# Optimization experiments

Measured on AMD Instinct MI355X. Metric: run time of the kernel, lower is better.

Reference implementation:

```python
import jax, jax.numpy as jnp
import numpy as np

B, T, D, H = 4, 2048, 1024, 16
HD = D // H  # head_dim = 64


def setup_inputs() -> dict:
    key = jax.random.key(0)
    ks = jax.random.split(key, 5)
    s = 0.02
    return {
        "x": jax.random.normal(ks[0], (B, T, D), dtype=jnp.float32),
        "Wq": jax.random.normal(ks[1], (D, D), dtype=jnp.float32) * s,
        "Wk": jax.random.normal(ks[2], (D, D), dtype=jnp.float32) * s,
        "Wv": jax.random.normal(ks[3], (D, D), dtype=jnp.float32) * s,
        "Wp": jax.random.normal(ks[4], (D, D), dtype=jnp.float32) * s,
    }


def reference(x, Wq, Wk, Wv, Wp):
    b, t, d = x.shape
    # QKV projections (bias=False), reshape to (b, h, t, hd)
    q = (x @ Wq.T).reshape(b, t, H, HD).transpose(0, 2, 1, 3)
    k = (x @ Wk.T).reshape(b, t, H, HD).transpose(0, 2, 1, 3)
    v = (x @ Wv.T).reshape(b, t, H, HD).transpose(0, 2, 1, 3)
    # scaled scores with causal mask
    scores = jnp.einsum("bhqd,bhkd->bhqk", q, k) / jnp.sqrt(jnp.float32(HD))
    causal = jnp.triu(jnp.ones((t, t), dtype=bool), k=1)
    scores = jnp.where(causal, -jnp.inf, scores)
    weights = jax.nn.softmax(scores, axis=-1)
    # dropout = 0.0 / eval mode -> identity
    ctx = jnp.einsum("bhqk,bhkd->bhqd", weights, v)
    ctx = ctx.transpose(0, 2, 1, 3).reshape(b, t, d)
    return ctx @ Wp.T
```

## Files before the change

kernel.cpp:

```cpp
#include <hip/hip_runtime.h>

typedef unsigned short u16;
typedef unsigned int u32;
typedef __attribute__((ext_vector_type(8))) short short8;
typedef __attribute__((ext_vector_type(4))) short short4_t;
typedef __attribute__((ext_vector_type(4))) float float4_t;

#define T_SEQ 2048
#define DMODEL 1024
#define NH 16
#define HD 64
#define NEG_BIG (-3.0e4f)

#define GLL16(g, l) __builtin_amdgcn_global_load_lds( \
    (const __attribute__((address_space(1))) u32*)(g), \
    (__attribute__((address_space(3))) u32*)(l), 16, 0, 0)

__device__ inline u16 f2b(float f) {
  u32 x = __builtin_bit_cast(u32, f);
  x += 0x7fffu + ((x >> 16) & 1u);
  return (u16)(x >> 16);
}

__global__ __launch_bounds__(256) void conv_f2b(
    const float* __restrict__ x, const float* __restrict__ wq,
    const float* __restrict__ wk, const float* __restrict__ wv,
    const float* __restrict__ wp, u16* __restrict__ xb, u16* __restrict__ wb) {
  const size_t SZc = (size_t)8192 * 1024, WSZc = (size_t)1024 * 1024;
  size_t i = ((size_t)blockIdx.x * 256 + threadIdx.x) * 8;
  const float* s; u16* d; size_t off;
  if (i < SZc) { s = x; d = xb; off = i; }
  else {
    size_t j = i - SZc;
    size_t w = j >> 20;
    off = j & (WSZc - 1);
    s = (w == 0) ? wq : (w == 1) ? wk : (w == 2) ? wv : wp;
    d = wb + w * WSZc;
  }
  float4_t a = *(const float4_t*)(s + off);
  float4_t b = *(const float4_t*)(s + off + 4);
  short8 o;
  o[0] = (short)f2b(a[0]); o[1] = (short)f2b(a[1]);
  o[2] = (short)f2b(a[2]); o[3] = (short)f2b(a[3]);
  o[4] = (short)f2b(b[0]); o[5] = (short)f2b(b[1]);
  o[6] = (short)f2b(b[2]); o[7] = (short)f2b(b[3]);
  *(short8*)(d + off) = o;
}

__global__ __launch_bounds__(256) void gemm_bt(
    const u16* __restrict__ A,
    const u16* __restrict__ B0, const u16* __restrict__ B1, const u16* __restrict__ B2,
    u16* __restrict__ C0, u16* __restrict__ C1, u16* __restrict__ C2,
    float* __restrict__ Cf,
    int N, int Kd, int vtz, int of32, int scz, float cscale)
{
  const u16* Bp = (blockIdx.z == 0) ? B0 : ((blockIdx.z == 1) ? B1 : B2);
  u16* Cp = (blockIdx.z == 0) ? C0 : ((blockIdx.z == 1) ? C1 : C2);
  const bool vt = ((int)blockIdx.z == vtz);
  const float cs = ((int)blockIdx.z == scz) ? cscale : 1.0f;
  __shared__ u16 As[128 * 32];
  __shared__ u16 Bs[128 * 32];
  const int tid = threadIdx.x;
  const int lane = tid & 63;
  const int li = lane & 15;
  const int quad = lane >> 4;
  const int wv = tid >> 6;
  const int wm = (wv >> 1) * 64;
  const int wn = (wv & 1) * 64;
  const size_t bm = (size_t)blockIdx.x * 128;
  const size_t bn = (size_t)blockIdx.y * 128;

  float4_t acc[4][4];
  const float4_t z4 = {0.f, 0.f, 0.f, 0.f};
#pragma unroll
  for (int i = 0; i < 4; i++)
#pragma unroll
    for (int j = 0; j < 4; j++) acc[i][j] = z4;

  const int c0 = tid, c1 = tid + 256;
  const int r0 = c0 >> 2, e0 = (c0 & 3) * 8;
  const int r1 = c1 >> 2, e1 = (c1 & 3) * 8;

  for (int k0 = 0; k0 < Kd; k0 += 32) {
    __syncthreads();
    GLL16(A + (bm + r0) * Kd + k0 + e0, &As[c0 * 8]);
    GLL16(A + (bm + r1) * Kd + k0 + e1, &As[c1 * 8]);
    GLL16(Bp + (bn + r0) * Kd + k0 + e0, &Bs[c0 * 8]);
    GLL16(Bp + (bn + r1) * Kd + k0 + e1, &Bs[c1 * 8]);
    __syncthreads();
    short8 af[4], bf[4];
#pragma unroll
    for (int i = 0; i < 4; i++)
      af[i] = *(const short8*)&As[(wm + i * 16 + li) * 32 + quad * 8];
#pragma unroll
    for (int j = 0; j < 4; j++)
      bf[j] = *(const short8*)&Bs[(wn + j * 16 + li) * 32 + quad * 8];
#pragma unroll
    for (int i = 0; i < 4; i++)
#pragma unroll
      for (int j = 0; j < 4; j++)
        acc[i][j] = __builtin_amdgcn_mfma_f32_16x16x32_bf16(af[i], bf[j], acc[i][j], 0, 0, 0);
  }

  if (of32) {
#pragma unroll
    for (int i = 0; i < 4; i++)
#pragma unroll
      for (int j = 0; j < 4; j++) {
        size_t row = bm + wm + (size_t)(i * 16 + quad * 4);
        size_t col = bn + wn + (size_t)(j * 16 + li);
#pragma unroll
        for (int r = 0; r < 4; r++)
          Cf[(row + r) * (size_t)N + col] = acc[i][j][r];
      }
  } else if (!vt) {
#pragma unroll
    for (int i = 0; i < 4; i++)
#pragma unroll
      for (int j = 0; j < 4; j++) {
        size_t row = bm + wm + (size_t)(i * 16 + quad * 4);
        size_t col = bn + wn + (size_t)(j * 16 + li);
#pragma unroll
        for (int r = 0; r < 4; r++)
          Cp[(row + r) * (size_t)N + col] = f2b(acc[i][j][r] * cs);
      }
  } else {
#pragma unroll
    for (int i = 0; i < 4; i++)
#pragma unroll
      for (int j = 0; j < 4; j++) {
        size_t row = bm + wm + (size_t)(i * 16 + quad * 4);
        size_t col = bn + wn + (size_t)(j * 16 + li);
        size_t bb = row >> 11;
        size_t tt = row & 2047;
        short4_t o;
#pragma unroll
        for (int r = 0; r < 4; r++) o[r] = (short)f2b(acc[i][j][r]);
        *(short4_t*)&Cp[(bb * 1024 + col) * 2048 + tt] = o;
      }
  }
}

#define LROW 72
__global__ __launch_bounds__(512) void attn_fwd(const u16* __restrict__ Qb,
                                                const u16* __restrict__ Kb,
                                                const u16* __restrict__ Vtb,
                                                u16* __restrict__ Ob) {
  __shared__ u16 Qs[128 * LROW];
  __shared__ u16 Ks[64 * LROW];
  __shared__ u16 Vs[64 * LROW];
  const int bh = blockIdx.y;
  const int bidx = bh >> 4;
  const int tid = threadIdx.x;
  const int lane = tid & 63;
  const int wv = tid >> 6;
  const int li = lane & 15;
  const int quad = lane >> 4;
  const size_t qkBase = ((size_t)bidx * T_SEQ) * DMODEL + (size_t)(bh & 15) * HD;
  const size_t vBase = (size_t)bh * HD * T_SEQ;
  const int krow = tid >> 3;
  const int kc8 = (tid & 7) * 8;
  const float4_t z4 = {0.f, 0.f, 0.f, 0.f};

#pragma unroll 1
  for (int ph = 0; ph < 2; ph++) {
    const int qblk = ph ? (int)blockIdx.x : (15 - (int)blockIdx.x);
    const int q0 = qblk * 128;

#pragma unroll
    for (int t = 0; t < 4; t++) {
      int slot = tid + t * 512;
      int row = slot >> 4, hc = slot & 15;
      *(short4_t*)&Qs[row * LROW + hc * 4] =
          *(const short4_t*)&Qb[qkBase + (size_t)(q0 + row) * DMODEL + hc * 4];
    }
    __syncthreads();
    short8 qf[2];
    {
      const int row = wv * 16 + li;
#pragma unroll
      for (int s = 0; s < 2; s++)
        qf[s] = *(const short8*)&Qs[row * LROW + s * 32 + quad * 8];
    }

    float4_t accO[4];
#pragma unroll
    for (int dt = 0; dt < 4; dt++) accO[dt] = z4;
    float l_i = 0.f;
    const int ktmax = 2 * qblk + 1;
    const int qg0 = q0 + wv * 16;

    short8 kpre = *(const short8*)&Kb[qkBase + (size_t)krow * DMODEL + kc8];
    short8 vpre = *(const short8*)&Vtb[vBase + (size_t)krow * T_SEQ + kc8];

    for (int kt = 0; kt <= ktmax; kt++) {
      const int k0 = kt * 64;
      __syncthreads();
      *(short8*)&Ks[krow * LROW + kc8] = kpre;
      *(short8*)&Vs[krow * LROW + kc8] = vpre;
      __syncthreads();
      if (kt < ktmax) {
        const int kn = k0 + 64;
        kpre = *(const short8*)&Kb[qkBase + (size_t)(kn + krow) * DMODEL + kc8];
        vpre = *(const short8*)&Vtb[vBase + (size_t)krow * T_SEQ + kn + kc8];
      }
      if (k0 > qg0 + 15) continue;

      float4_t st[4];
#pragma unroll
      for (int jt = 0; jt < 4; jt++) {
        float4_t c4 = z4;
        const int row = jt * 16 + li;
#pragma unroll
        for (int s = 0; s < 2; s++) {
          short8 kf = *(const short8*)&Ks[row * LROW + s * 32 + quad * 8];
          c4 = __builtin_amdgcn_mfma_f32_16x16x32_bf16(kf, qf[s], c4, 0, 0, 0);
        }
        st[jt] = c4;
      }

      float psum = 0.f;
      short4_t pf[4];
      if (k0 + 63 > qg0) {
        const int ig = qg0 + li;
#pragma unroll
        for (int jt = 0; jt < 4; jt++)
#pragma unroll
          for (int r = 0; r < 4; r++) {
            int jg = k0 + jt * 16 + quad * 4 + r;
            float p = (jg <= ig) ? __builtin_amdgcn_exp2f(st[jt][r]) : 0.f;
            psum += p;
            pf[jt][r] = (short)(__builtin_bit_cast(u32, p) >> 16);
          }
      } else {
#pragma unroll
        for (int jt = 0; jt < 4; jt++)
#pragma unroll
          for (int r = 0; r < 4; r++) {
            float p = __builtin_amdgcn_exp2f(st[jt][r]);
            psum += p;
            pf[jt][r] = (short)(__builtin_bit_cast(u32, p) >> 16);
          }
      }
      psum += __shfl_xor(psum, 16);
      psum += __shfl_xor(psum, 32);
      l_i += psum;

#pragma unroll
      for (int dt = 0; dt < 4; dt++) {
        const int d = dt * 16 + li;
#pragma unroll
        for (int jt = 0; jt < 4; jt++) {
          short4_t vf = *(const short4_t*)&Vs[d * LROW + jt * 16 + quad * 4];
          accO[dt] = __builtin_amdgcn_mfma_f32_16x16x16bf16_1k(vf, pf[jt], accO[dt], 0, 0, 0);
        }
      }
    }

    const float inv = 1.f / l_i;
    const int orow = q0 + wv * 16 + li;
    const size_t obase = ((size_t)bidx * T_SEQ + orow) * DMODEL + (size_t)(bh & 15) * HD;
#pragma unroll
    for (int dt = 0; dt < 4; dt++) {
      short4_t o4;
#pragma unroll
      for (int r = 0; r < 4; r++) o4[r] = (short)f2b(accO[dt][r] * inv);
      *(short4_t*)&Ob[obase + dt * 16 + quad * 4] = o4;
    }
  }
}

extern "C" void kernel_launch(void* const* d_in, const int* in_sizes, int n_in,
                              void* d_out, int out_size, void* d_ws, size_t ws_size,
                              hipStream_t stream) {
  (void)in_sizes; (void)n_in; (void)out_size; (void)ws_size;
  const float* x  = (const float*)d_in[0];
  const float* Wq = (const float*)d_in[1];
  const float* Wk = (const float*)d_in[2];
  const float* Wv = (const float*)d_in[3];
  const float* Wp = (const float*)d_in[4];
  float* out = (float*)d_out;

  const size_t SZ  = (size_t)8192 * 1024;
  const size_t WSZ = (size_t)1024 * 1024;

  u16* xb  = (u16*)d_ws;
  u16* wb  = xb + SZ;
  u16* Q   = wb + 4 * WSZ;
  u16* Kp  = Q + SZ;
  u16* Vt  = Kp + SZ;
  u16* ctx = Vt + SZ;

  const float SC = 0.18033688011112042f;

  dim3 blk(256);
  conv_f2b<<<dim3((unsigned)((SZ + 4 * WSZ) / 8 / 256)), blk, 0, stream>>>(
      x, Wq, Wk, Wv, Wp, xb, wb);
  gemm_bt<<<dim3(64, 8, 3), blk, 0, stream>>>(
      xb, wb, wb + WSZ, wb + 2 * WSZ, Q, Kp, Vt, nullptr, DMODEL, DMODEL, 2, 0,
      0, SC);
  attn_fwd<<<dim3(8, 4 * NH), dim3(512), 0, stream>>>(Q, Kp, Vt, ctx);
  gemm_bt<<<dim3(64, 8, 1), blk, 0, stream>>>(
      ctx, wb + 3 * WSZ, nullptr, nullptr, nullptr, nullptr, nullptr, out,
      DMODEL, DMODEL, -1, 1, -1, 1.0f);
}
```

Measured before the change: 256.2 us.

## Double-buffer K/V tiles in LDS and defer row-sum shuffle reduction

The attention kernel now keeps two LDS buffers for K and V tiles. The next tile is written into the alternate buffer while the current one is consumed, which removes one of the two block barriers per key-tile iteration. The per-iteration cross-lane shuffle reduction of the softmax denominator is also moved out of the loop and done once before normalization. The cost is double the K/V shared memory footprint, which could lower occupancy, plus an extra prologue load stage per phase.

```diff
diff --git a/kernel.cpp b/kernel.cpp
--- a/kernel.cpp
+++ b/kernel.cpp
@@ -10,7 +10,6 @@
 #define DMODEL 1024
 #define NH 16
 #define HD 64
-#define NEG_BIG (-3.0e4f)
 
 #define GLL16(g, l) __builtin_amdgcn_global_load_lds( \
     (const __attribute__((address_space(1))) u32*)(g), \
@@ -147,8 +146,8 @@
                                                 const u16* __restrict__ Vtb,
                                                 u16* __restrict__ Ob) {
   __shared__ u16 Qs[128 * LROW];
-  __shared__ u16 Ks[64 * LROW];
-  __shared__ u16 Vs[64 * LROW];
+  __shared__ u16 Kds[2][64 * LROW];
+  __shared__ u16 Vds[2][64 * LROW];
   const int bh = blockIdx.y;
   const int bidx = bh >> 4;
   const int tid = threadIdx.x;
@@ -160,13 +159,17 @@
   const size_t vBase = (size_t)bh * HD * T_SEQ;
   const int krow = tid >> 3;
   const int kc8 = (tid & 7) * 8;
+  const int kld = krow * LROW + kc8;
   const float4_t z4 = {0.f, 0.f, 0.f, 0.f};
 
 #pragma unroll 1
   for (int ph = 0; ph < 2; ph++) {
     const int qblk = ph ? (int)blockIdx.x : (15 - (int)blockIdx.x);
     const int q0 = qblk * 128;
-
+    const int ktmax = 2 * qblk + 1;
+    const int qg0 = q0 + wv * 16;
+
+    __syncthreads();
 #pragma unroll
     for (int t = 0; t < 4; t++) {
       int slot = tid + t * 512;
@@ -174,6 +177,8 @@
       *(short4_t*)&Qs[row * LROW + hc * 4] =
           *(const short4_t*)&Qb[qkBase + (size_t)(q0 + row) * DMODEL + hc * 4];
     }
+    short8 kpre = *(const short8*)&Kb[qkBase + (size_t)krow * DMODEL + kc8];
+    short8 vpre = *(const short8*)&Vtb[vBase + (size_t)krow * T_SEQ + kc8];
     __syncthreads();
     short8 qf[2];
     {
@@ -182,27 +187,28 @@
       for (int s = 0; s < 2; s++)
         qf[s] = *(const short8*)&Qs[row * LROW + s * 32 + quad * 8];
     }
+    *(short8*)&Kds[0][kld] = kpre;
+    *(short8*)&Vds[0][kld] = vpre;
+    kpre = *(const short8*)&Kb[qkBase + (size_t)(64 + krow) * DMODEL + kc8];
+    vpre = *(const short8*)&Vtb[vBase + (size_t)krow * T_SEQ + 64 + kc8];
 
     float4_t accO[4];
 #pragma unroll
     for (int dt = 0; dt < 4; dt++) accO[dt] = z4;
     float l_i = 0.f;
-    const int ktmax = 2 * qblk + 1;
-    const int qg0 = q0 + wv * 16;
-
-    short8 kpre = *(const short8*)&Kb[qkBase + (size_t)krow * DMODEL + kc8];
-    short8 vpre = *(const short8*)&Vtb[vBase + (size_t)krow * T_SEQ + kc8];
 
     for (int kt = 0; kt <= ktmax; kt++) {
       const int k0 = kt * 64;
-      __syncthreads();
-      *(short8*)&Ks[krow * LROW + kc8] = kpre;
-      *(short8*)&Vs[krow * LROW + kc8] = vpre;
+      const int cb = kt & 1;
       __syncthreads();
       if (kt < ktmax) {
-        const int kn = k0 + 64;
-        kpre = *(const short8*)&Kb[qkBase + (size_t)(kn + krow) * DMODEL + kc8];
-        vpre = *(const short8*)&Vtb[vBase + (size_t)krow * T_SEQ + kn + kc8];
+        *(short8*)&Kds[cb ^ 1][kld] = kpre;
+        *(short8*)&Vds[cb ^ 1][kld] = vpre;
+        if (kt + 1 < ktmax) {
+          const int kn = k0 + 128;
+          kpre = *(const short8*)&Kb[qkBase + (size_t)(kn + krow) * DMODEL + kc8];
+          vpre = *(const short8*)&Vtb[vBase + (size_t)krow * T_SEQ + kn + kc8];
+        }
       }
       if (k0 > qg0 + 15) continue;
 
@@ -213,13 +219,12 @@
         const int row = jt * 16 + li;
 #pragma unroll
         for (int s = 0; s < 2; s++) {
-          short8 kf = *(const short8*)&Ks[row * LROW + s * 32 + quad * 8];
+          short8 kf = *(const short8*)&Kds[cb][row * LROW + s * 32 + quad * 8];
           c4 = __builtin_amdgcn_mfma_f32_16x16x32_bf16(kf, qf[s], c4, 0, 0, 0);
         }
         st[jt] = c4;
       }
 
-      float psum = 0.f;
       short4_t pf[4];
       if (k0 + 63 > qg0) {
         const int ig = qg0 + li;
@@ -229,7 +234,7 @@
           for (int r = 0; r < 4; r++) {
             int jg = k0 + jt * 16 + quad * 4 + r;
             float p = (jg <= ig) ? __builtin_amdgcn_exp2f(st[jt][r]) : 0.f;
-            psum += p;
+            l_i += p;
             pf[jt][r] = (short)(__builtin_bit_cast(u32, p) >> 16);
           }
       } else {
@@ -238,25 +243,24 @@
 #pragma unroll
           for (int r = 0; r < 4; r++) {
             float p = __builtin_amdgcn_exp2f(st[jt][r]);
-            psum += p;
+            l_i += p;
             pf[jt][r] = (short)(__builtin_bit_cast(u32, p) >> 16);
           }
       }
-      psum += __shfl_xor(psum, 16);
-      psum += __shfl_xor(psum, 32);
-      l_i += psum;
 
 #pragma unroll
       for (int dt = 0; dt < 4; dt++) {
         const int d = dt * 16 + li;
 #pragma unroll
         for (int jt = 0; jt < 4; jt++) {
-          short4_t vf = *(const short4_t*)&Vs[d * LROW + jt * 16 + quad * 4];
+          short4_t vf = *(const short4_t*)&Vds[cb][d * LROW + jt * 16 + quad * 4];
           accO[dt] = __builtin_amdgcn_mfma_f32_16x16x16bf16_1k(vf, pf[jt], accO[dt], 0, 0, 0);
         }
       }
     }
 
+    l_i += __shfl_xor(l_i, 16);
+    l_i += __shfl_xor(l_i, 32);
     const float inv = 1.f / l_i;
     const int orow = q0 + wv * 16 + li;
     const size_t obase = ((size_t)bidx * T_SEQ + orow) * DMODEL + (size_t)(bh & 15) * HD;
```

Result: no change. 254.2 us (-0.8%).
